# Kernel optimization log

Hardware: AMD Instinct MI355X
Metric: run time of the kernel (lower is better)

The kernel has to match this reference:

```python
import jax, jax.numpy as jnp
import numpy as np

N = 100000       # nodes
E = 1600000      # edges (before self loops)
F_IN = 128       # num_node_features
D = 64           # conv_dim == label_dimension
G = 64           # global_dim
NG = 64          # num_graphs in batch


def _lin(key, fi, fo):
    kw, kb = jax.random.split(key)
    w = (jax.random.normal(kw, (fi, fo)) / np.float32(np.sqrt(fi))).astype(jnp.float32)
    b = (jax.random.normal(kb, (fo,)) * 0.01).astype(jnp.float32)
    return w, b


def setup_inputs() -> dict:
    key = jax.random.key(0)
    ks = jax.random.split(key, 12)
    x = jax.random.normal(ks[0], (N, F_IN), jnp.float32)
    edge_index = jax.random.randint(ks[1], (2, E), 0, N, dtype=jnp.int32)
    graph_indices = jnp.sort(jax.random.randint(ks[2], (N,), 0, NG, dtype=jnp.int32))
    glob_init = jax.random.normal(ks[3], (1, G), jnp.float32)
    w_nn1, b_nn1 = _lin(ks[4], F_IN, D)
    w_gn1, b_gn1 = _lin(ks[5], G, D)
    w_gg1, b_gg1 = _lin(ks[6], G, G)
    w_ng1, b_ng1 = _lin(ks[7], D, G)
    w_nn2, b_nn2 = _lin(ks[8], D, D)
    w_gn2, b_gn2 = _lin(ks[9], G, D)
    w_gg2, b_gg2 = _lin(ks[10], G, G)
    w_ng2, b_ng2 = _lin(ks[11], D, G)
    return dict(x=x, edge_index=edge_index, graph_indices=graph_indices,
                glob_init=glob_init,
                w_nn1=w_nn1, b_nn1=b_nn1, w_gn1=w_gn1, b_gn1=b_gn1,
                w_gg1=w_gg1, b_gg1=b_gg1, w_ng1=w_ng1, b_ng1=b_ng1,
                w_nn2=w_nn2, b_nn2=b_nn2, w_gn2=w_gn2, b_gn2=b_gn2,
                w_gg2=w_gg2, b_gg2=b_gg2, w_ng2=w_ng2, b_ng2=b_ng2)


def _gcn_glob_layer(xn, glob, row, col, graph_indices, params):
    # GCNConv_glob.forward. row/col already include self loops.
    w_nn, b_nn, w_gn, b_gn, w_gg, b_gg, w_ng, b_ng = params
    h = xn @ w_nn + b_nn                                   # [N, out]
    globs = glob @ w_gn + b_gn                             # [NG, out]
    # binary_matrix @ globs == one-hot gather by graph id
    h = h + globs[graph_indices]
    n = h.shape[0]
    deg = jax.ops.segment_sum(jnp.ones_like(col, dtype=h.dtype), col, num_segments=n)
    dinv = jnp.where(deg > 0, deg, 1.0) ** -0.5
    dinv = jnp.where(deg > 0, dinv, 0.0)
    norm = dinv[row] * dinv[col]                           # [E+N]
    msg = norm[:, None] * h[row]                           # gather + scale
    h = jax.ops.segment_sum(msg, col, num_segments=n)      # scatter-add
    glob2 = glob @ w_gg + b_gg
    parts = jax.ops.segment_max(h, graph_indices, num_segments=NG,
                                indices_are_sorted=True)   # scatter-max readout
    glob2 = glob2 + parts @ w_ng + b_ng
    return h, glob2


def reference(x, edge_index, graph_indices, glob_init,
              w_nn1, b_nn1, w_gn1, b_gn1, w_gg1, b_gg1, w_ng1, b_ng1,
              w_nn2, b_nn2, w_gn2, b_gn2, w_gg2, b_gg2, w_ng2, b_ng2):
    n = x.shape[0]
    loops = jnp.arange(n, dtype=edge_index.dtype)
    row = jnp.concatenate([edge_index[0], loops])          # add_self_loops
    col = jnp.concatenate([edge_index[1], loops])
    glob = jnp.tile(glob_init, (NG, 1))
    h, glob = _gcn_glob_layer(x, glob, row, col, graph_indices,
                              (w_nn1, b_nn1, w_gn1, b_gn1, w_gg1, b_gg1, w_ng1, b_ng1))
    h = jax.nn.relu(h)
    h, glob = _gcn_glob_layer(h, glob, row, col, graph_indices,
                              (w_nn2, b_nn2, w_gn2, b_gn2, w_gg2, b_gg2, w_ng2, b_ng2))
    return jax.nn.sigmoid(h)
```

## Files before the change

kernel.cpp:

```cpp
#include <hip/hip_runtime.h>
#include <math.h>

#define NN 100000
#define EE 1600000
#define FIN 128
#define DD 64
#define NG 64
#define NBINS ((NN + 255) / 256)
#define CH 8192
#define CAP 4608

typedef unsigned int uint;
typedef unsigned short ushort;

__device__ __forceinline__ unsigned f2ord(float f) {
  unsigned u = __float_as_uint(f);
  return (u & 0x80000000u) ? ~u : (u | 0x80000000u);
}
__device__ __forceinline__ float ord2f(unsigned m) {
  unsigned u = (m & 0x80000000u) ? (m & 0x7FFFFFFFu) : ~m;
  return __uint_as_float(u);
}
__device__ __forceinline__ float bflo(uint v) { return __uint_as_float(v << 16); }
__device__ __forceinline__ float bfhi(uint v) { return __uint_as_float(v & 0xffff0000u); }
__device__ __forceinline__ uint bfr(float x) {
  uint u = __float_as_uint(x);
  return (u + 0x7fffu + ((u >> 16) & 1u)) >> 16;
}
__device__ __forceinline__ uint packbf(float lo, float hi) { return bfr(lo) | (bfr(hi) << 16); }

__global__ __launch_bounds__(256) void pass1_bin(const int* __restrict__ row,
    const int* __restrict__ col, int* __restrict__ bcnt,
    uint* __restrict__ temp, uint* __restrict__ parts, int e) {
  __shared__ int hist[NBINS];
  __shared__ int base[NBINS];
  int tid = threadIdx.x;
  int s = blockIdx.x * CH;
  int colr[32];
  ushort rank[32];
  #pragma unroll
  for (int it = 0; it < 32; ++it) {
    int i = s + tid + it * 256;
    colr[it] = (i < e) ? __builtin_nontemporal_load(&col[i]) : -1;
  }
  if (blockIdx.x == 0)
    for (int i = tid; i < NG * 64; i += 256) parts[i] = 0u;
  for (int i = tid; i < NBINS; i += 256) hist[i] = 0;
  __syncthreads();
  #pragma unroll
  for (int it = 0; it < 32; ++it)
    if (colr[it] >= 0)
      rank[it] = (ushort)atomicAdd(&hist[colr[it] >> 8], 1);
  __syncthreads();
  for (int i = tid; i < NBINS; i += 256) {
    int cnt = hist[i];
    base[i] = cnt ? atomicAdd(&bcnt[i], cnt) : 0;
  }
  __syncthreads();
  #pragma unroll
  for (int it = 0; it < 32; ++it) {
    int c = colr[it];
    if (c >= 0) {
      int i = s + tid + it * 256;
      int r = __builtin_nontemporal_load(&row[i]);
      int b = c >> 8;
      int pos = base[b] + (int)rank[it];
      if (pos < CAP)
        temp[(size_t)b * CAP + pos] = ((uint)r << 8) | (uint)(c & 255);
    }
  }
}

__global__ __launch_bounds__(256) void pass2_scatter(const uint* __restrict__ temp,
    const int* __restrict__ bcnt, int* __restrict__ cursor0,
    int* __restrict__ deg, float* __restrict__ dinv,
    int* __restrict__ csr, int n) {
  __shared__ uint slice[CAP];
  __shared__ int hist[256];
  __shared__ int sc[256];
  int b = blockIdx.x;
  int tid = threadIdx.x;
  int cnt = bcnt[b]; if (cnt > CAP) cnt = CAP;
  const uint* tp = temp + (size_t)b * CAP;
  hist[tid] = 0;
  __syncthreads();
  for (int i = tid; i < cnt; i += 256) {
    uint rec = __builtin_nontemporal_load(&tp[i]);
    uint rk = (uint)atomicAdd(&hist[rec & 255u], 1);
    slice[i] = rec | (rk << 25);
  }
  __syncthreads();
  int v = hist[tid];
  sc[tid] = v;
  __syncthreads();
  for (int off = 1; off < 256; off <<= 1) {
    int t = (tid >= off) ? sc[tid - off] : 0;
    __syncthreads();
    sc[tid] += t;
    __syncthreads();
  }
  int st = b * CAP + sc[tid] - v;
  int node = b * 256 + tid;
  if (node < n) {
    cursor0[node] = st;
    deg[node] = v;
    dinv[node] = rsqrtf((float)v + 1.0f);
  }
  hist[tid] = st;
  __syncthreads();
  for (int i = tid; i < cnt; i += 256) {
    uint rec = slice[i];
    int lo = rec & 255u;
    int rk = rec >> 25;
    int src = (rec >> 8) & 0x1FFFF;
    csr[hist[lo] + rk] = src;
  }
}

__global__ __launch_bounds__(256) void gemm1(const float* __restrict__ x,
    const float* __restrict__ w, const float* __restrict__ b,
    const float* __restrict__ gi, const float* __restrict__ w_gn1,
    const float* __restrict__ b_gn1, const float* __restrict__ dinv,
    uint* __restrict__ hbf, int n) {
  __shared__ float XsT[64][128];
  __shared__ float Ws[64][DD];
  __shared__ float g1s[64];
  int tid = threadIdx.x;
  int base = blockIdx.x * 128;
  if (blockIdx.x == 0 && tid >= 64 && tid < 96)
    hbf[(size_t)n * 32 + (tid - 64)] = 0u;
  if (tid < 64) {
    float a = b_gn1[tid];
    for (int k = 0; k < 64; ++k) a += gi[k] * w_gn1[k * 64 + tid];
    g1s[tid] = a;
  }
  int tx = tid & 15, ty = tid >> 4;
  float acc[8][4] = {};
  const float4* x4 = (const float4*)x;
  const float4* w4 = (const float4*)w;
  #pragma unroll
  for (int c = 0; c < 2; ++c) {
    __syncthreads();
    for (int idx = tid; idx < 1024; idx += 256)
      ((float4*)Ws)[idx] = w4[c * 1024 + idx];
    for (int idx = tid; idx < 2048; idx += 256) {
      int kq = idx & 15, r = idx >> 4;
      int gr = base + r;
      float4 v = make_float4(0.f, 0.f, 0.f, 0.f);
      if (gr < n) v = x4[(size_t)gr * 32 + c * 16 + kq];
      int k0 = kq * 4, s = k0 & 60;
      XsT[k0 + 0][r ^ s] = v.x;
      XsT[k0 + 1][r ^ s] = v.y;
      XsT[k0 + 2][r ^ s] = v.z;
      XsT[k0 + 3][r ^ s] = v.w;
    }
    __syncthreads();
    #pragma unroll 4
    for (int k = 0; k < 64; ++k) {
      int s = k & 60;
      float4 alo = *(const float4*)&XsT[k][(8 * ty) ^ s];
      float4 ahi = *(const float4*)&XsT[k][(8 * ty + 4) ^ s];
      float4 bv  = *(const float4*)&Ws[k][4 * tx];
      float ax[8] = {alo.x, alo.y, alo.z, alo.w, ahi.x, ahi.y, ahi.z, ahi.w};
      float bx[4] = {bv.x, bv.y, bv.z, bv.w};
      #pragma unroll
      for (int i = 0; i < 8; ++i)
        #pragma unroll
        for (int j = 0; j < 4; ++j)
          acc[i][j] += ax[i] * bx[j];
    }
  }
  float bias[4];
  #pragma unroll
  for (int j = 0; j < 4; ++j) bias[j] = b[4 * tx + j] + g1s[4 * tx + j];
  #pragma unroll
  for (int i = 0; i < 8; ++i) {
    int row = base + 8 * ty + i;
    if (row < n) {
      float dv = dinv[row];
      hbf[(size_t)row * 32 + 2 * tx]     = packbf(dv * (acc[i][0] + bias[0]), dv * (acc[i][1] + bias[1]));
      hbf[(size_t)row * 32 + 2 * tx + 1] = packbf(dv * (acc[i][2] + bias[2]), dv * (acc[i][3] + bias[3]));
    }
  }
}

__global__ __launch_bounds__(256) void gemm2(const uint* __restrict__ hbf,
    const float* __restrict__ w, const float* __restrict__ bb,
    const float* __restrict__ globs2, const int* __restrict__ gidx,
    const float* __restrict__ dinv, uint* __restrict__ obf, int n) {
  __shared__ float XsT[64][128];
  __shared__ float Ws[64][DD];
  int tid = threadIdx.x;
  int base = blockIdx.x * 128;
  const float4* w4 = (const float4*)w;
  for (int idx = tid; idx < 1024; idx += 256)
    ((float4*)Ws)[idx] = w4[idx];
  const uint2* h2 = (const uint2*)hbf;
  for (int idx = tid; idx < 2048; idx += 256) {
    int kq = idx & 15, r = idx >> 4;
    int gr = base + r;
    uint2 v = make_uint2(0u, 0u);
    if (gr < n) v = h2[(size_t)gr * 16 + kq];
    int k0 = kq * 4, s = k0 & 60;
    XsT[k0 + 0][r ^ s] = fmaxf(bflo(v.x), 0.f);
    XsT[k0 + 1][r ^ s] = fmaxf(bfhi(v.x), 0.f);
    XsT[k0 + 2][r ^ s] = fmaxf(bflo(v.y), 0.f);
    XsT[k0 + 3][r ^ s] = fmaxf(bfhi(v.y), 0.f);
  }
  int tx = tid & 15, ty = tid >> 4;
  __syncthreads();
  float acc[8][4] = {};
  #pragma unroll 4
  for (int k = 0; k < 64; ++k) {
    int s = k & 60;
    float4 alo = *(const float4*)&XsT[k][(8 * ty) ^ s];
    float4 ahi = *(const float4*)&XsT[k][(8 * ty + 4) ^ s];
    float4 bv  = *(const float4*)&Ws[k][4 * tx];
    float ax[8] = {alo.x, alo.y, alo.z, alo.w, ahi.x, ahi.y, ahi.z, ahi.w};
    float bx[4] = {bv.x, bv.y, bv.z, bv.w};
    #pragma unroll
    for (int i = 0; i < 8; ++i)
      #pragma unroll
      for (int j = 0; j < 4; ++j)
        acc[i][j] += ax[i] * bx[j];
  }
  #pragma unroll
  for (int i = 0; i < 8; ++i) {
    int row = base + 8 * ty + i;
    if (row < n) {
      const float* gl = globs2 + gidx[row] * 64 + 4 * tx;
      float dv = dinv[row];
      float c0 = acc[i][0] + bb[4 * tx + 0] + gl[0];
      float c1 = acc[i][1] + bb[4 * tx + 1] + gl[1];
      float c2 = acc[i][2] + bb[4 * tx + 2] + gl[2];
      float c3 = acc[i][3] + bb[4 * tx + 3] + gl[3];
      obf[(size_t)row * 32 + 2 * tx]     = packbf(dv * c0, dv * c1);
      obf[(size_t)row * 32 + 2 * tx + 1] = packbf(dv * c2, dv * c3);
    }
  }
}

template <int SIG>
__global__ __launch_bounds__(256) void gather_agg(const int* __restrict__ csr,
    const int* __restrict__ cursor0, const int* __restrict__ deg,
    const float* __restrict__ dinv, const uint* __restrict__ h,
    void* __restrict__ outv, int n) {
  int node = blockIdx.x * 4 + (threadIdx.x >> 6);
  if (node >= n) return;
  int lane = threadIdx.x & 63;
  int q = lane >> 4;
  int fq = lane & 15;
  int start = cursor0[node];
  int end = start + deg[node];
  int last = end - 1;
  const uint2* h2 = (const uint2*)h;
  float a0 = 0.f, a1 = 0.f, a2 = 0.f, a3 = 0.f;
  for (int e = start + q; e < end; e += 16) {
    #pragma unroll
    for (int j = 0; j < 4; ++j) {
      int i = e + 4 * j;
      int ic = i < last ? i : last;
      int r = __builtin_nontemporal_load(&csr[ic]);
      r = (i < end) ? r : n;
      uint2 v = h2[(size_t)r * 16 + fq];
      a0 += bflo(v.x); a1 += bfhi(v.x);
      a2 += bflo(v.y); a3 += bfhi(v.y);
    }
  }
  if (q == 0) {
    uint2 v = h2[(size_t)node * 16 + fq];
    a0 += bflo(v.x); a1 += bfhi(v.x);
    a2 += bflo(v.y); a3 += bfhi(v.y);
  }
  a0 += __shfl_xor(a0, 16); a0 += __shfl_xor(a0, 32);
  a1 += __shfl_xor(a1, 16); a1 += __shfl_xor(a1, 32);
  a2 += __shfl_xor(a2, 16); a2 += __shfl_xor(a2, 32);
  a3 += __shfl_xor(a3, 16); a3 += __shfl_xor(a3, 32);
  if (q == 0) {
    float di = dinv[node];
    a0 *= di; a1 *= di; a2 *= di; a3 *= di;
    if (SIG) {
      float4 o;
      o.x = 1.f / (1.f + __expf(-a0));
      o.y = 1.f / (1.f + __expf(-a1));
      o.z = 1.f / (1.f + __expf(-a2));
      o.w = 1.f / (1.f + __expf(-a3));
      ((float4*)outv)[(size_t)node * 16 + fq] = o;
    } else {
      uint2 o;
      o.x = packbf(a0, a1);
      o.y = packbf(a2, a3);
      ((uint2*)outv)[(size_t)node * 16 + fq] = o;
    }
  }
}

__global__ __launch_bounds__(256) void seg_max(const uint* __restrict__ B,
    const int* __restrict__ gidx, unsigned* __restrict__ parts_ord, int n) {
  int f2 = threadIdx.x & 31;
  int sub = threadIdx.x >> 5;
  int start = blockIdx.x * 128 + sub * 16;
  if (start >= n) return;
  int end = start + 16; if (end > n) end = n;
  int curg = gidx[start];
  float m0 = -INFINITY, m1 = -INFINITY;
  for (int i = start; i < end; ++i) {
    int g = gidx[i];
    if (g != curg) {
      atomicMax(&parts_ord[curg * 64 + 2 * f2],     f2ord(m0));
      atomicMax(&parts_ord[curg * 64 + 2 * f2 + 1], f2ord(m1));
      curg = g; m0 = -INFINITY; m1 = -INFINITY;
    }
    uint v = B[(size_t)i * 32 + f2];
    m0 = fmaxf(m0, bflo(v));
    m1 = fmaxf(m1, bfhi(v));
  }
  atomicMax(&parts_ord[curg * 64 + 2 * f2],     f2ord(m0));
  atomicMax(&parts_ord[curg * 64 + 2 * f2 + 1], f2ord(m1));
}

__global__ void glob2_kernel(const float* __restrict__ gi, const unsigned* __restrict__ parts_ord,
    const float* __restrict__ w_gg1, const float* __restrict__ b_gg1,
    const float* __restrict__ w_ng1, const float* __restrict__ b_ng1,
    const float* __restrict__ w_gn2, const float* __restrict__ b_gn2,
    float* __restrict__ globs2) {
  __shared__ float t[64];
  int g = blockIdx.x, j = threadIdx.x;
  float acc = b_gg1[j] + b_ng1[j];
  for (int k = 0; k < 64; ++k) acc += gi[k] * w_gg1[k * 64 + j];
  for (int k = 0; k < 64; ++k) acc += ord2f(parts_ord[g * 64 + k]) * w_ng1[k * 64 + j];
  t[j] = acc;
  __syncthreads();
  float acc2 = b_gn2[j];
  for (int k = 0; k < 64; ++k) acc2 += t[k] * w_gn2[k * 64 + j];
  globs2[g * 64 + j] = acc2;
}

extern "C" void kernel_launch(void* const* d_in, const int* in_sizes, int n_in,
                              void* d_out, int out_size, void* d_ws, size_t ws_size,
                              hipStream_t stream) {
  const float* x         = (const float*)d_in[0];
  const int*   ei        = (const int*)d_in[1];
  const int*   gidx      = (const int*)d_in[2];
  const float* glob_init = (const float*)d_in[3];
  const float* w_nn1 = (const float*)d_in[4];  const float* b_nn1 = (const float*)d_in[5];
  const float* w_gn1 = (const float*)d_in[6];  const float* b_gn1 = (const float*)d_in[7];
  const float* w_gg1 = (const float*)d_in[8];  const float* b_gg1 = (const float*)d_in[9];
  const float* w_ng1 = (const float*)d_in[10]; const float* b_ng1 = (const float*)d_in[11];
  const float* w_nn2 = (const float*)d_in[12]; const float* b_nn2 = (const float*)d_in[13];
  const float* w_gn2 = (const float*)d_in[14]; const float* b_gn2 = (const float*)d_in[15];

  const int* row = ei;
  const int* col = ei + EE;

  char* p = (char*)d_ws;
  int*      deg    = (int*)p;       p += ((NN * 4 + 255) & ~255);
  float*    dinv   = (float*)p;     p += ((NN * 4 + 255) & ~255);
  int*      cursor = (int*)p;       p += ((NN * 4 + 255) & ~255);
  int*      bcnt   = (int*)p;       p += ((NBINS * 4 + 255) & ~255);
  uint*     temp   = (uint*)p;      p += (size_t)NBINS * CAP * 4;
  int*      csr    = (int*)p;       p += (size_t)NBINS * CAP * 4;
  uint*     A      = (uint*)p;      p += (size_t)(NN + 1) * 32 * 4;
  unsigned* parts  = (unsigned*)p;  p += NG * 64 * 4;
  float*    globs2 = (float*)p;
  uint*     B      = (uint*)d_out;
  float*    out    = (float*)d_out;

  hipMemsetAsync(bcnt, 0, NBINS * 4, stream);
  pass1_bin<<<(EE + CH - 1) / CH, 256, 0, stream>>>(row, col, bcnt, temp, parts, EE);
  pass2_scatter<<<NBINS, 256, 0, stream>>>(temp, bcnt, cursor, deg, dinv, csr, NN);

  gemm1<<<(NN + 127) / 128, 256, 0, stream>>>(x, w_nn1, b_nn1, glob_init, w_gn1, b_gn1,
                                              dinv, A, NN);
  gather_agg<0><<<(NN + 3) / 4, 256, 0, stream>>>(csr, cursor, deg, dinv, A, (void*)B, NN);

  seg_max<<<(NN + 127) / 128, 256, 0, stream>>>(B, gidx, parts, NN);
  glob2_kernel<<<NG, 64, 0, stream>>>(glob_init, parts, w_gg1, b_gg1, w_ng1, b_ng1,
                                      w_gn2, b_gn2, globs2);

  gemm2<<<(NN + 127) / 128, 256, 0, stream>>>(B, w_nn2, b_nn2, globs2, gidx, dinv, A, NN);
  gather_agg<1><<<(NN + 3) / 4, 256, 0, stream>>>(csr, cursor, deg, dinv, A, (void*)out, NN);
}
```

Measured before the change: 248.9 us.

## Use bf16 MFMA in gemm2, fuse glob update into it, privatize pass1 histograms

gemm2 now computes its tile with bf16 MFMA 16x16x32 instructions. Its A operand is read directly from the bf16 buffer, with ReLU applied by bit masking, and the weights are repacked to bf16 in shared memory. The separate glob2 kernel is removed: each gemm2 block recomputes the global-feature projection for the up to 8 graphs its 128 rows span, trading redundant small matmuls for one fewer launch. pass1_bin spreads its shared histogram across 4 sub-copies to cut LDS atomic contention. Quantizing the weights to bf16 and capping each block at 8 graphs add some precision and correctness risk.

```diff
diff --git a/kernel.cpp b/kernel.cpp
--- a/kernel.cpp
+++ b/kernel.cpp
@@ -12,6 +12,10 @@
 
 typedef unsigned int uint;
 typedef unsigned short ushort;
+typedef __attribute__((ext_vector_type(8))) short s8v;
+typedef __attribute__((ext_vector_type(4))) float f32x4;
+
+union U16B { uint4 u4; s8v s; };
 
 __device__ __forceinline__ unsigned f2ord(float f) {
   unsigned u = __float_as_uint(f);
@@ -28,13 +32,18 @@
   return (u + 0x7fffu + ((u >> 16) & 1u)) >> 16;
 }
 __device__ __forceinline__ uint packbf(float lo, float hi) { return bfr(lo) | (bfr(hi) << 16); }
+__device__ __forceinline__ uint relu2(uint v) {
+  uint m = ((v >> 15) & 0x10001u) * 0xFFFFu;
+  return v & ~m;
+}
 
 __global__ __launch_bounds__(256) void pass1_bin(const int* __restrict__ row,
     const int* __restrict__ col, int* __restrict__ bcnt,
     uint* __restrict__ temp, uint* __restrict__ parts, int e) {
-  __shared__ int hist[NBINS];
-  __shared__ int base[NBINS];
+  __shared__ int hist[4][NBINS];
+  __shared__ int base[4][NBINS];
   int tid = threadIdx.x;
+  int sub = tid & 3;
   int s = blockIdx.x * CH;
   int colr[32];
   ushort rank[32];
@@ -45,16 +54,21 @@
   }
   if (blockIdx.x == 0)
     for (int i = tid; i < NG * 64; i += 256) parts[i] = 0u;
-  for (int i = tid; i < NBINS; i += 256) hist[i] = 0;
+  for (int i = tid; i < 4 * NBINS; i += 256) (&hist[0][0])[i] = 0;
   __syncthreads();
   #pragma unroll
   for (int it = 0; it < 32; ++it)
     if (colr[it] >= 0)
-      rank[it] = (ushort)atomicAdd(&hist[colr[it] >> 8], 1);
+      rank[it] = (ushort)atomicAdd(&hist[sub][colr[it] >> 8], 1);
   __syncthreads();
   for (int i = tid; i < NBINS; i += 256) {
-    int cnt = hist[i];
-    base[i] = cnt ? atomicAdd(&bcnt[i], cnt) : 0;
+    int h0 = hist[0][i], h1 = hist[1][i], h2 = hist[2][i], h3 = hist[3][i];
+    int tot = h0 + h1 + h2 + h3;
+    int b = tot ? atomicAdd(&bcnt[i], tot) : 0;
+    base[0][i] = b;
+    base[1][i] = b + h0;
+    base[2][i] = b + h0 + h1;
+    base[3][i] = b + h0 + h1 + h2;
   }
   __syncthreads();
   #pragma unroll
@@ -64,7 +78,7 @@
       int i = s + tid + it * 256;
       int r = __builtin_nontemporal_load(&row[i]);
       int b = c >> 8;
-      int pos = base[b] + (int)rank[it];
+      int pos = base[sub][b] + (int)rank[it];
       if (pos < CAP)
         temp[(size_t)b * CAP + pos] = ((uint)r << 8) | (uint)(c & 255);
     }
@@ -186,56 +200,88 @@
 
 __global__ __launch_bounds__(256) void gemm2(const uint* __restrict__ hbf,
     const float* __restrict__ w, const float* __restrict__ bb,
-    const float* __restrict__ globs2, const int* __restrict__ gidx,
-    const float* __restrict__ dinv, uint* __restrict__ obf, int n) {
-  __shared__ float XsT[64][128];
-  __shared__ float Ws[64][DD];
+    const int* __restrict__ gidx, const float* __restrict__ dinv,
+    const unsigned* __restrict__ parts_ord, const float* __restrict__ gi,
+    const float* __restrict__ w_gg1, const float* __restrict__ b_gg1,
+    const float* __restrict__ w_ng1, const float* __restrict__ b_ng1,
+    const float* __restrict__ w_gn2, const float* __restrict__ b_gn2,
+    uint* __restrict__ obf, int n) {
+  __shared__ uint  Wt[64 * 36];
+  __shared__ float t1L[8 * 64];
+  __shared__ float globsL[8 * 64];
+  __shared__ float Cst[128 * 65];
   int tid = threadIdx.x;
-  int base = blockIdx.x * 128;
-  const float4* w4 = (const float4*)w;
-  for (int idx = tid; idx < 1024; idx += 256)
-    ((float4*)Ws)[idx] = w4[idx];
-  const uint2* h2 = (const uint2*)hbf;
-  for (int idx = tid; idx < 2048; idx += 256) {
-    int kq = idx & 15, r = idx >> 4;
-    int gr = base + r;
-    uint2 v = make_uint2(0u, 0u);
-    if (gr < n) v = h2[(size_t)gr * 16 + kq];
-    int k0 = kq * 4, s = k0 & 60;
-    XsT[k0 + 0][r ^ s] = fmaxf(bflo(v.x), 0.f);
-    XsT[k0 + 1][r ^ s] = fmaxf(bfhi(v.x), 0.f);
-    XsT[k0 + 2][r ^ s] = fmaxf(bflo(v.y), 0.f);
-    XsT[k0 + 3][r ^ s] = fmaxf(bfhi(v.y), 0.f);
-  }
-  int tx = tid & 15, ty = tid >> 4;
-  __syncthreads();
-  float acc[8][4] = {};
-  #pragma unroll 4
-  for (int k = 0; k < 64; ++k) {
-    int s = k & 60;
-    float4 alo = *(const float4*)&XsT[k][(8 * ty) ^ s];
-    float4 ahi = *(const float4*)&XsT[k][(8 * ty + 4) ^ s];
-    float4 bv  = *(const float4*)&Ws[k][4 * tx];
-    float ax[8] = {alo.x, alo.y, alo.z, alo.w, ahi.x, ahi.y, ahi.z, ahi.w};
-    float bx[4] = {bv.x, bv.y, bv.z, bv.w};
+  int blockBase = blockIdx.x * 128;
+  int rlast = blockBase + 127; if (rlast >= n) rlast = n - 1;
+  int g0 = gidx[blockBase];
+  int g1 = gidx[rlast];
+  int ng = g1 - g0 + 1; if (ng > 8) ng = 8;
+  for (int idx = tid; idx < 64 * 32; idx += 256) {
+    int j = idx >> 5, kp = idx & 31;
+    Wt[j * 36 + kp] = packbf(w[(2 * kp) * 64 + j], w[(2 * kp + 1) * 64 + j]);
+  }
+  for (int idx = tid; idx < ng * 64; idx += 256) {
+    int gg = idx >> 6, j = idx & 63;
+    float a = b_gg1[j] + b_ng1[j];
+    for (int k = 0; k < 64; ++k) a += gi[k] * w_gg1[k * 64 + j];
+    const unsigned* pr = parts_ord + (size_t)(g0 + gg) * 64;
+    for (int k = 0; k < 64; ++k) a += ord2f(pr[k]) * w_ng1[k * 64 + j];
+    t1L[idx] = a;
+  }
+  __syncthreads();
+  for (int idx = tid; idx < ng * 64; idx += 256) {
+    int gg = idx >> 6, j = idx & 63;
+    float a = b_gn2[j];
+    const float* t1 = t1L + gg * 64;
+    for (int k = 0; k < 64; ++k) a += t1[k] * w_gn2[k * 64 + j];
+    globsL[idx] = a;
+  }
+  __syncthreads();
+  int wv = tid >> 6, lane = tid & 63;
+  int li = lane & 15, lc = lane >> 4;
+  int rb = blockBase + wv * 32;
+  f32x4 acc[2][4] = {};
+  const uint4* b4 = (const uint4*)hbf;
+  #pragma unroll
+  for (int ks = 0; ks < 2; ++ks) {
+    s8v afr[2];
     #pragma unroll
-    for (int i = 0; i < 8; ++i)
+    for (int m = 0; m < 2; ++m) {
+      int row = rb + m * 16 + li;
+      bool valid = row < n;
+      int rc = valid ? row : (n - 1);
+      uint4 v = b4[(size_t)rc * 8 + ks * 4 + lc];
+      if (!valid) v = make_uint4(0u, 0u, 0u, 0u);
+      v.x = relu2(v.x); v.y = relu2(v.y); v.z = relu2(v.z); v.w = relu2(v.w);
+      U16B u; u.u4 = v; afr[m] = u.s;
+    }
+    #pragma unroll
+    for (int c = 0; c < 4; ++c) {
+      int j = c * 16 + li;
+      U16B u; u.u4 = *(const uint4*)&Wt[j * 36 + ks * 16 + lc * 4];
       #pragma unroll
-      for (int j = 0; j < 4; ++j)
-        acc[i][j] += ax[i] * bx[j];
-  }
-  #pragma unroll
-  for (int i = 0; i < 8; ++i) {
-    int row = base + 8 * ty + i;
+      for (int m = 0; m < 2; ++m)
+        acc[m][c] = __builtin_amdgcn_mfma_f32_16x16x32_bf16(afr[m], u.s, acc[m][c], 0, 0, 0);
+    }
+  }
+  #pragma unroll
+  for (int m = 0; m < 2; ++m)
+    #pragma unroll
+    for (int c = 0; c < 4; ++c)
+      #pragma unroll
+      for (int r = 0; r < 4; ++r)
+        Cst[(wv * 32 + m * 16 + lc * 4 + r) * 65 + c * 16 + li] = acc[m][c][r];
+  __syncthreads();
+  for (int idx = tid; idx < 128 * 32; idx += 256) {
+    int r = idx >> 5, us = idx & 31;
+    int row = blockBase + r;
     if (row < n) {
-      const float* gl = globs2 + gidx[row] * 64 + 4 * tx;
+      int c0 = us * 2, c1 = c0 + 1;
+      int gg = gidx[row] - g0; if (gg > 7) gg = 7;
       float dv = dinv[row];
-      float c0 = acc[i][0] + bb[4 * tx + 0] + gl[0];
-      float c1 = acc[i][1] + bb[4 * tx + 1] + gl[1];
-      float c2 = acc[i][2] + bb[4 * tx + 2] + gl[2];
-      float c3 = acc[i][3] + bb[4 * tx + 3] + gl[3];
-      obf[(size_t)row * 32 + 2 * tx]     = packbf(dv * c0, dv * c1);
-      obf[(size_t)row * 32 + 2 * tx + 1] = packbf(dv * c2, dv * c3);
+      float v0 = Cst[r * 65 + c0] + bb[c0] + globsL[gg * 64 + c0];
+      float v1 = Cst[r * 65 + c1] + bb[c1] + globsL[gg * 64 + c1];
+      obf[(size_t)row * 32 + us] = packbf(dv * v0, dv * v1);
     }
   }
 }
@@ -319,23 +365,6 @@
   atomicMax(&parts_ord[curg * 64 + 2 * f2 + 1], f2ord(m1));
 }
 
-__global__ void glob2_kernel(const float* __restrict__ gi, const unsigned* __restrict__ parts_ord,
-    const float* __restrict__ w_gg1, const float* __restrict__ b_gg1,
-    const float* __restrict__ w_ng1, const float* __restrict__ b_ng1,
-    const float* __restrict__ w_gn2, const float* __restrict__ b_gn2,
-    float* __restrict__ globs2) {
-  __shared__ float t[64];
-  int g = blockIdx.x, j = threadIdx.x;
-  float acc = b_gg1[j] + b_ng1[j];
-  for (int k = 0; k < 64; ++k) acc += gi[k] * w_gg1[k * 64 + j];
-  for (int k = 0; k < 64; ++k) acc += ord2f(parts_ord[g * 64 + k]) * w_ng1[k * 64 + j];
-  t[j] = acc;
-  __syncthreads();
-  float acc2 = b_gn2[j];
-  for (int k = 0; k < 64; ++k) acc2 += t[k] * w_gn2[k * 64 + j];
-  globs2[g * 64 + j] = acc2;
-}
-
 extern "C" void kernel_launch(void* const* d_in, const int* in_sizes, int n_in,
                               void* d_out, int out_size, void* d_ws, size_t ws_size,
                               hipStream_t stream) {
@@ -362,7 +391,6 @@
   int*      csr    = (int*)p;       p += (size_t)NBINS * CAP * 4;
   uint*     A      = (uint*)p;      p += (size_t)(NN + 1) * 32 * 4;
   unsigned* parts  = (unsigned*)p;  p += NG * 64 * 4;
-  float*    globs2 = (float*)p;
   uint*     B      = (uint*)d_out;
   float*    out    = (float*)d_out;
 
@@ -375,9 +403,9 @@
   gather_agg<0><<<(NN + 3) / 4, 256, 0, stream>>>(csr, cursor, deg, dinv, A, (void*)B, NN);
 
   seg_max<<<(NN + 127) / 128, 256, 0, stream>>>(B, gidx, parts, NN);
-  glob2_kernel<<<NG, 64, 0, stream>>>(glob_init, parts, w_gg1, b_gg1, w_ng1, b_ng1,
-                                      w_gn2, b_gn2, globs2);
-
-  gemm2<<<(NN + 127) / 128, 256, 0, stream>>>(B, w_nn2, b_nn2, globs2, gidx, dinv, A, NN);
+
+  gemm2<<<(NN + 127) / 128, 256, 0, stream>>>(B, w_nn2, b_nn2, gidx, dinv, parts,
+                                              glob_init, w_gg1, b_gg1, w_ng1, b_ng1,
+                                              w_gn2, b_gn2, A, NN);
   gather_agg<1><<<(NN + 3) / 4, 256, 0, stream>>>(csr, cursor, deg, dinv, A, (void*)out, NN);
 }
```

After: 249.9 us. About the same (+0.4%).
